# Kernel optimization log

Measured on AMD Instinct MI355X. Metric: run time of the kernel, lower is better.

Reference implementation:

```python
import jax, jax.numpy as jnp
import numpy as np

N_NODES = 50000   # local subgraph nodes
N_ENT   = 100000  # global entity vocab
N_REL   = 16
DIM     = 128
LAYERS  = 2
E       = 600000  # edges
Q       = 8192    # query triples
PATH_DIM = 5
RULE_INIT = [[1.0, 1.0, 0.5, 0.0, 0.0], [0.0, 0.0, 0.0, 1.0, 1.0]]


def setup_inputs() -> dict:
    key = jax.random.key(0)
    ks = jax.random.split(key, 11)
    node_ids   = jax.random.randint(ks[0], (N_NODES,), 0, N_ENT)
    edge_index = jax.random.randint(ks[1], (2, E), 0, N_NODES)
    edge_type  = jax.random.randint(ks[2], (E,), 0, N_REL)
    heads = jax.random.randint(ks[3], (Q,), 0, N_NODES)
    rels  = jax.random.randint(ks[4], (Q,), 0, N_REL)
    tails = jax.random.randint(ks[5], (Q,), 0, N_NODES)
    path_feat = jax.random.normal(ks[6], (Q, PATH_DIM), dtype=jnp.float32)
    # learned parameters
    entity_emb = jax.random.normal(ks[7], (N_ENT, DIM), dtype=jnp.float32) * 0.1
    rel_emb    = jax.random.normal(ks[8], (N_REL, DIM), dtype=jnp.float32) * 0.1
    W_self = jax.random.normal(ks[9], (LAYERS, DIM, DIM), dtype=jnp.float32) / np.sqrt(DIM)
    W_rel  = jax.random.normal(ks[10], (LAYERS, N_REL, DIM, DIM), dtype=jnp.float32) / np.sqrt(DIM)
    delta_weight = jnp.zeros((2, PATH_DIM), dtype=jnp.float32)
    lambda_logit = jnp.zeros((2,), dtype=jnp.float32)
    rule_init_weight = jnp.asarray(RULE_INIT, dtype=jnp.float32)
    return {
        'node_ids': node_ids, 'edge_index': edge_index, 'edge_type': edge_type,
        'heads': heads, 'rels': rels, 'tails': tails,
        'path_feat': path_feat, 'rel_task_idx': 0,
        'entity_emb': entity_emb, 'rel_emb': rel_emb,
        'W_self': W_self, 'W_rel': W_rel,
        'delta_weight': delta_weight, 'lambda_logit': lambda_logit,
        'rule_init_weight': rule_init_weight,
    }


def _rgcn_layer(h, Ws, Wr, src, dst, etype):
    # relation-specific transforms for all nodes: [R, N, D]
    h_rel = jnp.einsum('nd,rde->rne', h, Wr)
    msgs = h_rel[etype, src]                    # [E, D] gather per edge
    # per-(dst, relation) mean normalization (standard RGCN 1/c_{i,r})
    seg = dst * N_REL + etype
    cnt = jax.ops.segment_sum(jnp.ones((E,), h.dtype), seg, num_segments=N_NODES * N_REL)
    msgs = msgs / jnp.maximum(cnt[seg], 1.0)[:, None]
    agg = jax.ops.segment_sum(msgs, dst, num_segments=N_NODES)  # [N, D]
    return jax.nn.relu(h @ Ws + agg)


def reference(node_ids, edge_index, edge_type, heads, rels, tails, path_feat,
              rel_task_idx, entity_emb, rel_emb, W_self, W_rel,
              delta_weight, lambda_logit, rule_init_weight):
    src, dst = edge_index[0], edge_index[1]
    h = entity_emb[node_ids]                      # [N, D] local node states
    for l in range(LAYERS):
        h = _rgcn_layer(h, W_self[l], W_rel[l], src, dst, edge_type)
    # DistMult scoring of query triples (local indices)
    score_graph = jnp.sum(h[heads] * rel_emb[rels] * h[tails], axis=-1)  # [Q]
    # path branch
    final_weight = rule_init_weight[rel_task_idx] + delta_weight[rel_task_idx]  # [PATH_DIM]
    score_path = path_feat @ final_weight                                # [Q]
    lam = jax.nn.sigmoid(lambda_logit[rel_task_idx])
    return lam * score_graph + (1.0 - lam) * score_path
```

## Files before the change

### kernel.cpp

```cpp
#include <hip/hip_runtime.h>

#define N_NODES 50000
#define N_ENT   100000
#define N_REL   16
#define DIM     128
#define E_EDGES 600000
#define NQ      8192
#define PATH_DIM 5
#define NK      (N_NODES * N_REL)
#define NBLK_SEG (NK / 256)
#define KTOT    (N_REL * DIM + DIM)
#define NG      (KTOT / 32)
#define BM      64

typedef __attribute__((ext_vector_type(8))) short short8;
typedef __attribute__((ext_vector_type(4))) float floatx4;

static __device__ __forceinline__ short f2bf(float x) {
  unsigned u = __builtin_bit_cast(unsigned, x);
  u = (u + 0x7FFFu + ((u >> 16) & 1u)) >> 16;
  return (short)u;
}
static __device__ __forceinline__ float bf_lo(unsigned u) {
  return __builtin_bit_cast(float, u << 16);
}
static __device__ __forceinline__ float bf_hi(unsigned u) {
  return __builtin_bit_cast(float, u & 0xffff0000u);
}
static __device__ __forceinline__ unsigned pk2(float a, float b) {
  return (unsigned)(unsigned short)f2bf(a) | ((unsigned)(unsigned short)f2bf(b) << 16);
}

static __device__ __forceinline__ int wave_incl_scan(int x) {
  int lane = threadIdx.x & 63;
  #pragma unroll
  for (int off = 1; off < 64; off <<= 1) {
    int y = __shfl_up(x, off, 64);
    if (lane >= off) x += y;
  }
  return x;
}

__global__ void k_hist(const int* __restrict__ ei, const int* __restrict__ et,
                       int* __restrict__ hist) {
  int e = blockIdx.x * 256 + threadIdx.x;
  if (e >= E_EDGES) return;
  int key = et[e] * N_NODES + ei[E_EDGES + e];
  atomicAdd(&hist[key], 1);
}

__global__ void k_bsum(const int* __restrict__ hist, int* __restrict__ bsum) {
  int t = threadIdx.x;
  int v = hist[blockIdx.x * 256 + t];
  #pragma unroll
  for (int off = 32; off; off >>= 1) v += __shfl_xor(v, off, 64);
  __shared__ int s4[4];
  if ((t & 63) == 0) s4[t >> 6] = v;
  __syncthreads();
  if (t == 0) bsum[blockIdx.x] = s4[0] + s4[1] + s4[2] + s4[3];
}

__global__ void k_bscan(int* __restrict__ bsum) {
  int t = threadIdx.x;
  int v[4], loc[4], s = 0;
  #pragma unroll
  for (int i = 0; i < 4; i++) {
    int idx = t * 4 + i;
    v[i] = (idx < NBLK_SEG) ? bsum[idx] : 0;
    loc[i] = s; s += v[i];
  }
  int incl = wave_incl_scan(s);
  __shared__ int wsum[16];
  int wid = t >> 6, lane = t & 63;
  if (lane == 63) wsum[wid] = incl;
  __syncthreads();
  if (t < 16) {
    int x = wsum[t];
    #pragma unroll
    for (int off = 1; off < 16; off <<= 1) {
      int y = __shfl_up(x, off, 64);
      if (t >= off) x += y;
    }
    wsum[t] = x;
  }
  __syncthreads();
  int wexcl = wid ? wsum[wid - 1] : 0;
  int texcl = wexcl + incl - s;
  #pragma unroll
  for (int i = 0; i < 4; i++) {
    int idx = t * 4 + i;
    if (idx < NBLK_SEG) bsum[idx] = texcl + loc[i];
  }
}

__global__ void k_offsets(const int* __restrict__ hist, const int* __restrict__ bsum,
                          int* __restrict__ offs, int* __restrict__ cursor) {
  int t = threadIdx.x;
  int g = blockIdx.x * 256 + t;
  int v = hist[g];
  int incl = wave_incl_scan(v);
  __shared__ int wsum[4];
  int wid = t >> 6, lane = t & 63;
  if (lane == 63) wsum[wid] = incl;
  __syncthreads();
  int wexcl = 0;
  for (int i = 0; i < wid; i++) wexcl += wsum[i];
  int off = bsum[blockIdx.x] + wexcl + incl - v;
  offs[g] = off;
  cursor[g] = off;
  if (g == NK - 1) offs[NK] = off + v;
}

__global__ void k_scatter(const int* __restrict__ ei, const int* __restrict__ et,
                          int* __restrict__ cursor, int* __restrict__ ssrc) {
  int e = blockIdx.x * 256 + threadIdx.x;
  if (e >= E_EDGES) return;
  int src = ei[e];
  int key = et[e] * N_NODES + ei[E_EDGES + e];
  int pos = atomicAdd(&cursor[key], 1);
  ssrc[pos] = src;
}

__global__ void k_h0(const int* __restrict__ nid, const float* __restrict__ emb,
                     unsigned* __restrict__ h) {
  int g = blockIdx.x * 256 + threadIdx.x;
  int n = g >> 5;
  int q = g & 31;
  float4 v = *(const float4*)(emb + (size_t)nid[n] * DIM + q * 4);
  uint2 pk;
  pk.x = pk2(v.x, v.y);
  pk.y = pk2(v.z, v.w);
  *(uint2*)(h + (size_t)n * 64 + q * 2) = pk;
}

__global__ void k_wcat(const float* __restrict__ wrel, const float* __restrict__ wself,
                       short* __restrict__ wt) {
  int idx = blockIdx.x * 256 + threadIdx.x;
  if (idx >= 2 * NG * 8 * 512) return;
  int within = idx & 511;
  int tile = idx >> 9;
  int rA = within >> 5, q = within & 31;
  int nt8 = tile & 7;
  int lg = tile >> 3;
  int l = lg / NG, g = lg % NG;
  int n = nt8 * 16 + rA;
  int k = g * 32 + q;
  float v;
  if (k < N_REL * DIM) {
    int r = k >> 7, d = k & 127;
    v = wrel[(((size_t)l * N_REL + r) * DIM + d) * DIM + n];
  } else {
    int d = k - N_REL * DIM;
    v = wself[((size_t)l * DIM + d) * DIM + n];
  }
  wt[idx] = f2bf(v);
}

__global__ __launch_bounds__(512, 4) void k_layer(const unsigned* __restrict__ hin,
                                                  const int* __restrict__ offs,
                                                  const int* __restrict__ ssrc,
                                                  const short* __restrict__ wt,
                                                  const unsigned* __restrict__ zrow,
                                                  unsigned* __restrict__ hout) {
  __shared__ unsigned As[2][BM][68];
  __shared__ int offsS[16][66];
  int t = threadIdx.x;
  int w = t >> 6, lane = t & 63;
  int row0 = blockIdx.x * BM;

  for (int idx = t; idx < 16 * 80; idx += 512) {
    int it = idx / 80, r = idx - it * 80;
    if (r < 65) offsS[it][r] = offs[min(it * N_NODES + row0 + r, NK)];
  }
  __syncthreads();

  if (w < 4) {
    int pw = w;
    int seg = lane & 15, edge = lane >> 4;
    int s_l = offsS[0][pw * 16 + seg];
    int e_l = offsS[0][pw * 16 + seg + 1];
    int pfe = ssrc[min(s_l + edge, E_EDGES - 1)];

    auto produce = [&](int buf, int it) {
      int cl = e_l - s_l;
      float invl = 1.0f / (float)(cl > 0 ? cl : 1);
      int invb = __builtin_bit_cast(int, invl);
      unsigned u0[16], u1[16], u2[16], u3[16];
      #pragma unroll
      for (int j = 0; j < 16; ++j) {
        int cnt = __builtin_amdgcn_readlane(cl, j);
        int r0 = __builtin_amdgcn_readlane(pfe, j);
        int r1 = __builtin_amdgcn_readlane(pfe, j + 16);
        int r2 = __builtin_amdgcn_readlane(pfe, j + 32);
        int r3 = __builtin_amdgcn_readlane(pfe, j + 48);
        const unsigned* p0 = (cnt > 0) ? hin + (size_t)r0 * 64 : zrow;
        const unsigned* p1 = (cnt > 1) ? hin + (size_t)r1 * 64 : zrow;
        const unsigned* p2 = (cnt > 2) ? hin + (size_t)r2 * 64 : zrow;
        const unsigned* p3 = (cnt > 3) ? hin + (size_t)r3 * 64 : zrow;
        u0[j] = p0[lane];
        u1[j] = p1[lane];
        u2[j] = p2[lane];
        u3[j] = p3[lane];
      }
      int pfe_n = 0, s_n = 0, e_n = 0;
      if (it < 15) {
        s_n = offsS[it + 1][pw * 16 + seg];
        e_n = offsS[it + 1][pw * 16 + seg + 1];
        pfe_n = ssrc[min(s_n + edge, E_EDGES - 1)];
      }
      __builtin_amdgcn_sched_barrier(0);
      #pragma unroll
      for (int j = 0; j < 16; ++j) {
        int cnt = __builtin_amdgcn_readlane(cl, j);
        float inv = __builtin_bit_cast(float, __builtin_amdgcn_readlane(invb, j));
        float s0 = bf_lo(u0[j]) + bf_lo(u1[j]) + bf_lo(u2[j]) + bf_lo(u3[j]);
        float s1 = bf_hi(u0[j]) + bf_hi(u1[j]) + bf_hi(u2[j]) + bf_hi(u3[j]);
        if (cnt > 4) {
          int sj = __builtin_amdgcn_readlane(s_l, j);
          for (int p = sj + 4; p < sj + cnt; ++p) {
            int sr = __builtin_amdgcn_readfirstlane(ssrc[p]);
            unsigned uu = hin[(size_t)sr * 64 + lane];
            s0 += bf_lo(uu); s1 += bf_hi(uu);
          }
        }
        s0 *= inv; s1 *= inv;
        unsigned pk;
        asm("v_cvt_pk_bf16_f32 %0, %1, %2" : "=v"(pk) : "v"(s0), "v"(s1));
        As[buf][pw * 16 + j][lane] = pk;
      }
      s_l = s_n; e_l = e_n; pfe = pfe_n;
    };

    produce(0, 0);
    __syncthreads();
    for (int it = 0; it < 17; ++it) {
      int nx = it + 1;
      if (nx < 16) {
        produce(nx & 1, nx);
      } else if (nx == 16) {
        #pragma unroll
        for (int j = 0; j < 16; ++j) {
          int lr = min(row0 + pw * 16 + j, N_NODES - 1);
          As[0][pw * 16 + j][lane] = hin[(size_t)lr * 64 + lane];
        }
      }
      __syncthreads();
    }
  } else {
    int wid = w - 4, wm = wid >> 1, wn = wid & 1;
    int quad = lane >> 4, rA = lane & 15;
    floatx4 acc[2][4];
    #pragma unroll
    for (int a = 0; a < 2; a++)
      #pragma unroll
      for (int b = 0; b < 4; b++) acc[a][b] = (floatx4)0.f;

    __syncthreads();
    for (int it = 0; it < 17; ++it) {
      int buf = it & 1;
      const short* arow0 = (const short*)&As[buf][wm * 32 + rA][0];
      const short* arow1 = (const short*)&As[buf][wm * 32 + 16 + rA][0];
      #pragma unroll
      for (int ks = 0; ks < 4; ++ks) {
        short8 a0 = *(const short8*)(arow0 + ks * 32 + quad * 8);
        short8 a1 = *(const short8*)(arow1 + ks * 32 + quad * 8);
        int kg = it * 4 + ks;
        const short* bp = wt + (size_t)(kg * 8 + wn * 4) * 512 + rA * 32 + quad * 8;
        #pragma unroll
        for (int nt = 0; nt < 4; ++nt) {
          short8 b = *(const short8*)(bp + nt * 512);
          acc[0][nt] = __builtin_amdgcn_mfma_f32_16x16x32_bf16(a0, b, acc[0][nt], 0, 0, 0);
          acc[1][nt] = __builtin_amdgcn_mfma_f32_16x16x32_bf16(a1, b, acc[1][nt], 0, 0, 0);
        }
      }
      __syncthreads();
    }
    #pragma unroll
    for (int mt = 0; mt < 2; ++mt)
      #pragma unroll
      for (int nt = 0; nt < 4; ++nt)
        #pragma unroll
        for (int j = 0; j < 4; ++j) {
          int row = row0 + wm * 32 + mt * 16 + quad * 4 + j;
          int col = wn * 64 + nt * 16 + rA;
          if (row < N_NODES)
            ((short*)hout)[(size_t)row * DIM + col] = f2bf(fmaxf(acc[mt][nt][j], 0.f));
        }
  }
}

__global__ void k_score(const unsigned* __restrict__ h, const int* __restrict__ heads,
                        const int* __restrict__ rels, const int* __restrict__ tails,
                        const float* __restrict__ rel_emb, const float* __restrict__ path_feat,
                        const int* __restrict__ task_idx, const float* __restrict__ delta_w,
                        const float* __restrict__ lambda_logit, const float* __restrict__ rule_init,
                        float* __restrict__ out) {
  int q = (blockIdx.x * 256 + threadIdx.x) >> 6;
  int lane = threadIdx.x & 63;
  int hd = heads[q], tl = tails[q], rl = rels[q];
  unsigned ua = h[(size_t)hd * 64 + lane];
  unsigned uc = h[(size_t)tl * 64 + lane];
  float2 r = *(const float2*)(rel_emb + (size_t)rl * DIM + lane * 2);
  float s = bf_lo(ua) * r.x * bf_lo(uc) + bf_hi(ua) * r.y * bf_hi(uc);
  #pragma unroll
  for (int off = 32; off; off >>= 1) s += __shfl_xor(s, off, 64);
  if (lane == 0) {
    int task = task_idx[0];
    float sp = 0.f;
    #pragma unroll
    for (int p = 0; p < PATH_DIM; p++)
      sp += path_feat[q * PATH_DIM + p] *
            (rule_init[task * PATH_DIM + p] + delta_w[task * PATH_DIM + p]);
    float lam = 1.f / (1.f + __expf(-lambda_logit[task]));
    out[q] = lam * s + (1.f - lam) * sp;
  }
}

extern "C" void kernel_launch(void* const* d_in, const int* in_sizes, int n_in,
                              void* d_out, int out_size, void* d_ws, size_t ws_size,
                              hipStream_t stream) {
  const int*   node_ids   = (const int*)d_in[0];
  const int*   edge_index = (const int*)d_in[1];
  const int*   edge_type  = (const int*)d_in[2];
  const int*   heads      = (const int*)d_in[3];
  const int*   rels       = (const int*)d_in[4];
  const int*   tails      = (const int*)d_in[5];
  const float* path_feat  = (const float*)d_in[6];
  const int*   task_idx   = (const int*)d_in[7];
  const float* entity_emb = (const float*)d_in[8];
  const float* rel_emb    = (const float*)d_in[9];
  const float* W_self     = (const float*)d_in[10];
  const float* W_rel      = (const float*)d_in[11];
  const float* delta_w    = (const float*)d_in[12];
  const float* lambda_lg  = (const float*)d_in[13];
  const float* rule_init  = (const float*)d_in[14];

  char* ws = (char*)d_ws;
  size_t off = 0;
  auto alloc = [&](size_t bytes) -> void* {
    void* p = ws + off;
    off = (off + bytes + 255) & ~(size_t)255;
    return p;
  };
  unsigned* h_a    = (unsigned*)alloc((size_t)N_NODES * DIM * 2);
  unsigned* h_b    = (unsigned*)alloc((size_t)N_NODES * DIM * 2);
  short*    wt     = (short*)alloc((size_t)2 * NG * 8 * 512 * 2);
  int*      offs   = (int*)alloc((size_t)(NK + 1) * 4);
  int*      ssrc   = (int*)alloc((size_t)E_EDGES * 4);
  int*      hist   = (int*)alloc((size_t)(NK + 1) * 4);
  int*      cursor = (int*)alloc((size_t)NK * 4);
  int*      bsum   = (int*)alloc((size_t)NBLK_SEG * 4);
  unsigned* zrow   = (unsigned*)alloc(256);

  hipMemsetAsync(hist, 0, (size_t)(NK + 1) * 4, stream);
  hipMemsetAsync(zrow, 0, 256, stream);
  int eb = (E_EDGES + 255) / 256;
  k_hist<<<eb, 256, 0, stream>>>(edge_index, edge_type, hist);
  k_bsum<<<NBLK_SEG, 256, 0, stream>>>(hist, bsum);
  k_bscan<<<1, 1024, 0, stream>>>(bsum);
  k_offsets<<<NBLK_SEG, 256, 0, stream>>>(hist, bsum, offs, cursor);
  k_scatter<<<eb, 256, 0, stream>>>(edge_index, edge_type, cursor, ssrc);
  k_h0<<<(N_NODES * 32) / 256, 256, 0, stream>>>(node_ids, entity_emb, h_a);
  k_wcat<<<(2 * NG * 8 * 512 + 255) / 256, 256, 0, stream>>>(W_rel, W_self, wt);

  const unsigned* hin = h_a;
  unsigned* hout = h_b;
  int nblk = (N_NODES + BM - 1) / BM;
  for (int l = 0; l < 2; l++) {
    k_layer<<<nblk, 512, 0, stream>>>(hin, offs, ssrc,
                                      wt + (size_t)l * NG * 8 * 512, zrow, hout);
    const unsigned* tmp = hout;
    hout = (unsigned*)hin;
    hin = tmp;
  }
  k_score<<<NQ / 4, 256, 0, stream>>>(hin, heads, rels, tails, rel_emb, path_feat,
                                      task_idx, delta_w, lambda_lg, rule_init,
                                      (float*)d_out);
}
```

Measured before the change: 449.3 us.

## Replace CSR build with fixed 4-slot buckets plus overflow linked lists

The histogram, block-sum, scan, offsets and scatter kernels are replaced by a single bucketing kernel. Each (relation, dst) key gets four direct slots, and any further edges go into an atomically allocated overflow linked list. The layer kernel reads counts and slots directly, no longer stages offsets in shared memory, and skips the gathers for empty segments. This removes several preprocessing launches, at the cost of a larger slot array and serial pointer-chasing for high-degree keys. Summation order for overflow edges becomes nondeterministic.

```diff
diff --git a/kernel.cpp b/kernel.cpp
--- a/kernel.cpp
+++ b/kernel.cpp
@@ -8,7 +8,6 @@
 #define NQ      8192
 #define PATH_DIM 5
 #define NK      (N_NODES * N_REL)
-#define NBLK_SEG (NK / 256)
 #define KTOT    (N_REL * DIM + DIM)
 #define NG      (KTOT / 32)
 #define BM      64
@@ -31,94 +30,22 @@
   return (unsigned)(unsigned short)f2bf(a) | ((unsigned)(unsigned short)f2bf(b) << 16);
 }
 
-static __device__ __forceinline__ int wave_incl_scan(int x) {
-  int lane = threadIdx.x & 63;
-  #pragma unroll
-  for (int off = 1; off < 64; off <<= 1) {
-    int y = __shfl_up(x, off, 64);
-    if (lane >= off) x += y;
-  }
-  return x;
-}
-
-__global__ void k_hist(const int* __restrict__ ei, const int* __restrict__ et,
-                       int* __restrict__ hist) {
-  int e = blockIdx.x * 256 + threadIdx.x;
-  if (e >= E_EDGES) return;
-  int key = et[e] * N_NODES + ei[E_EDGES + e];
-  atomicAdd(&hist[key], 1);
-}
-
-__global__ void k_bsum(const int* __restrict__ hist, int* __restrict__ bsum) {
-  int t = threadIdx.x;
-  int v = hist[blockIdx.x * 256 + t];
-  #pragma unroll
-  for (int off = 32; off; off >>= 1) v += __shfl_xor(v, off, 64);
-  __shared__ int s4[4];
-  if ((t & 63) == 0) s4[t >> 6] = v;
-  __syncthreads();
-  if (t == 0) bsum[blockIdx.x] = s4[0] + s4[1] + s4[2] + s4[3];
-}
-
-__global__ void k_bscan(int* __restrict__ bsum) {
-  int t = threadIdx.x;
-  int v[4], loc[4], s = 0;
-  #pragma unroll
-  for (int i = 0; i < 4; i++) {
-    int idx = t * 4 + i;
-    v[i] = (idx < NBLK_SEG) ? bsum[idx] : 0;
-    loc[i] = s; s += v[i];
-  }
-  int incl = wave_incl_scan(s);
-  __shared__ int wsum[16];
-  int wid = t >> 6, lane = t & 63;
-  if (lane == 63) wsum[wid] = incl;
-  __syncthreads();
-  if (t < 16) {
-    int x = wsum[t];
-    #pragma unroll
-    for (int off = 1; off < 16; off <<= 1) {
-      int y = __shfl_up(x, off, 64);
-      if (t >= off) x += y;
-    }
-    wsum[t] = x;
-  }
-  __syncthreads();
-  int wexcl = wid ? wsum[wid - 1] : 0;
-  int texcl = wexcl + incl - s;
-  #pragma unroll
-  for (int i = 0; i < 4; i++) {
-    int idx = t * 4 + i;
-    if (idx < NBLK_SEG) bsum[idx] = texcl + loc[i];
-  }
-}
-
-__global__ void k_offsets(const int* __restrict__ hist, const int* __restrict__ bsum,
-                          int* __restrict__ offs, int* __restrict__ cursor) {
-  int t = threadIdx.x;
-  int g = blockIdx.x * 256 + t;
-  int v = hist[g];
-  int incl = wave_incl_scan(v);
-  __shared__ int wsum[4];
-  int wid = t >> 6, lane = t & 63;
-  if (lane == 63) wsum[wid] = incl;
-  __syncthreads();
-  int wexcl = 0;
-  for (int i = 0; i < wid; i++) wexcl += wsum[i];
-  int off = bsum[blockIdx.x] + wexcl + incl - v;
-  offs[g] = off;
-  cursor[g] = off;
-  if (g == NK - 1) offs[NK] = off + v;
-}
-
-__global__ void k_scatter(const int* __restrict__ ei, const int* __restrict__ et,
-                          int* __restrict__ cursor, int* __restrict__ ssrc) {
+__global__ void k_bucket(const int* __restrict__ ei, const int* __restrict__ et,
+                         int* __restrict__ cnt, int* __restrict__ head,
+                         int* __restrict__ cursor, int* __restrict__ slots,
+                         int* __restrict__ ovf_src, int* __restrict__ ovf_next) {
   int e = blockIdx.x * 256 + threadIdx.x;
   if (e >= E_EDGES) return;
   int src = ei[e];
   int key = et[e] * N_NODES + ei[E_EDGES + e];
-  int pos = atomicAdd(&cursor[key], 1);
-  ssrc[pos] = src;
+  int pos = atomicAdd(&cnt[key], 1);
+  if (pos < 4) {
+    slots[(size_t)key * 4 + pos] = src;
+  } else {
+    int nid = atomicAdd(cursor, 1) + 1;
+    ovf_src[nid] = src;
+    ovf_next[nid] = atomicExch(&head[key], nid);
+  }
 }
 
 __global__ void k_h0(const int* __restrict__ nid, const float* __restrict__ emb,
@@ -157,78 +84,81 @@
 }
 
 __global__ __launch_bounds__(512, 4) void k_layer(const unsigned* __restrict__ hin,
-                                                  const int* __restrict__ offs,
-                                                  const int* __restrict__ ssrc,
+                                                  const int* __restrict__ gcnt,
+                                                  const int* __restrict__ slots,
+                                                  const int* __restrict__ head,
+                                                  const int* __restrict__ ovf_src,
+                                                  const int* __restrict__ ovf_next,
                                                   const short* __restrict__ wt,
                                                   const unsigned* __restrict__ zrow,
                                                   unsigned* __restrict__ hout) {
   __shared__ unsigned As[2][BM][68];
-  __shared__ int offsS[16][66];
   int t = threadIdx.x;
   int w = t >> 6, lane = t & 63;
   int row0 = blockIdx.x * BM;
 
-  for (int idx = t; idx < 16 * 80; idx += 512) {
-    int it = idx / 80, r = idx - it * 80;
-    if (r < 65) offsS[it][r] = offs[min(it * N_NODES + row0 + r, NK)];
-  }
-  __syncthreads();
-
   if (w < 4) {
     int pw = w;
     int seg = lane & 15, edge = lane >> 4;
-    int s_l = offsS[0][pw * 16 + seg];
-    int e_l = offsS[0][pw * 16 + seg + 1];
-    int pfe = ssrc[min(s_l + edge, E_EDGES - 1)];
+    int segbase = row0 + pw * 16;
+    int k0 = min(segbase + seg, NK - 1);
+    int cl  = gcnt[k0];
+    int pfe = slots[(size_t)k0 * 4 + edge];
 
     auto produce = [&](int buf, int it) {
-      int cl = e_l - s_l;
       float invl = 1.0f / (float)(cl > 0 ? cl : 1);
       int invb = __builtin_bit_cast(int, invl);
       unsigned u0[16], u1[16], u2[16], u3[16];
       #pragma unroll
       for (int j = 0; j < 16; ++j) {
-        int cnt = __builtin_amdgcn_readlane(cl, j);
-        int r0 = __builtin_amdgcn_readlane(pfe, j);
-        int r1 = __builtin_amdgcn_readlane(pfe, j + 16);
-        int r2 = __builtin_amdgcn_readlane(pfe, j + 32);
-        int r3 = __builtin_amdgcn_readlane(pfe, j + 48);
-        const unsigned* p0 = (cnt > 0) ? hin + (size_t)r0 * 64 : zrow;
-        const unsigned* p1 = (cnt > 1) ? hin + (size_t)r1 * 64 : zrow;
-        const unsigned* p2 = (cnt > 2) ? hin + (size_t)r2 * 64 : zrow;
-        const unsigned* p3 = (cnt > 3) ? hin + (size_t)r3 * 64 : zrow;
-        u0[j] = p0[lane];
-        u1[j] = p1[lane];
-        u2[j] = p2[lane];
-        u3[j] = p3[lane];
-      }
-      int pfe_n = 0, s_n = 0, e_n = 0;
+        int cj = __builtin_amdgcn_readlane(cl, j);
+        if (cj > 0) {
+          int r0 = __builtin_amdgcn_readlane(pfe, j);
+          int r1 = __builtin_amdgcn_readlane(pfe, j + 16);
+          int r2 = __builtin_amdgcn_readlane(pfe, j + 32);
+          int r3 = __builtin_amdgcn_readlane(pfe, j + 48);
+          const unsigned* p1 = (cj > 1) ? hin + (size_t)r1 * 64 : zrow;
+          const unsigned* p2 = (cj > 2) ? hin + (size_t)r2 * 64 : zrow;
+          const unsigned* p3 = (cj > 3) ? hin + (size_t)r3 * 64 : zrow;
+          u0[j] = hin[(size_t)r0 * 64 + lane];
+          u1[j] = p1[lane];
+          u2[j] = p2[lane];
+          u3[j] = p3[lane];
+        }
+      }
+      int cl_n = 0, pfe_n = 0;
       if (it < 15) {
-        s_n = offsS[it + 1][pw * 16 + seg];
-        e_n = offsS[it + 1][pw * 16 + seg + 1];
-        pfe_n = ssrc[min(s_n + edge, E_EDGES - 1)];
+        int kn = min((it + 1) * N_NODES + segbase + seg, NK - 1);
+        cl_n = gcnt[kn];
+        pfe_n = slots[(size_t)kn * 4 + edge];
       }
       __builtin_amdgcn_sched_barrier(0);
       #pragma unroll
       for (int j = 0; j < 16; ++j) {
-        int cnt = __builtin_amdgcn_readlane(cl, j);
-        float inv = __builtin_bit_cast(float, __builtin_amdgcn_readlane(invb, j));
-        float s0 = bf_lo(u0[j]) + bf_lo(u1[j]) + bf_lo(u2[j]) + bf_lo(u3[j]);
-        float s1 = bf_hi(u0[j]) + bf_hi(u1[j]) + bf_hi(u2[j]) + bf_hi(u3[j]);
-        if (cnt > 4) {
-          int sj = __builtin_amdgcn_readlane(s_l, j);
-          for (int p = sj + 4; p < sj + cnt; ++p) {
-            int sr = __builtin_amdgcn_readfirstlane(ssrc[p]);
-            unsigned uu = hin[(size_t)sr * 64 + lane];
-            s0 += bf_lo(uu); s1 += bf_hi(uu);
+        int cj = __builtin_amdgcn_readlane(cl, j);
+        if (cj == 0) {
+          As[buf][pw * 16 + j][lane] = 0u;
+        } else {
+          float inv = __builtin_bit_cast(float, __builtin_amdgcn_readlane(invb, j));
+          float s0 = bf_lo(u0[j]) + bf_lo(u1[j]) + bf_lo(u2[j]) + bf_lo(u3[j]);
+          float s1 = bf_hi(u0[j]) + bf_hi(u1[j]) + bf_hi(u2[j]) + bf_hi(u3[j]);
+          if (cj > 4) {
+            int kj = min(it * N_NODES + segbase + j, NK - 1);
+            int cur = __builtin_amdgcn_readfirstlane(head[kj]);
+            for (int x = 4; x < cj; ++x) {
+              int sr = __builtin_amdgcn_readfirstlane(ovf_src[cur]);
+              unsigned uu = hin[(size_t)sr * 64 + lane];
+              s0 += bf_lo(uu); s1 += bf_hi(uu);
+              cur = __builtin_amdgcn_readfirstlane(ovf_next[cur]);
+            }
           }
-        }
-        s0 *= inv; s1 *= inv;
-        unsigned pk;
-        asm("v_cvt_pk_bf16_f32 %0, %1, %2" : "=v"(pk) : "v"(s0), "v"(s1));
-        As[buf][pw * 16 + j][lane] = pk;
-      }
-      s_l = s_n; e_l = e_n; pfe = pfe_n;
+          s0 *= inv; s1 *= inv;
+          unsigned pk;
+          asm("v_cvt_pk_bf16_f32 %0, %1, %2" : "=v"(pk) : "v"(s0), "v"(s1));
+          As[buf][pw * 16 + j][lane] = pk;
+        }
+      }
+      cl = cl_n; pfe = pfe_n;
     };
 
     produce(0, 0);
@@ -240,7 +170,7 @@
       } else if (nx == 16) {
         #pragma unroll
         for (int j = 0; j < 16; ++j) {
-          int lr = min(row0 + pw * 16 + j, N_NODES - 1);
+          int lr = min(segbase + j, N_NODES - 1);
           As[0][pw * 16 + j][lane] = hin[(size_t)lr * 64 + lane];
         }
       }
@@ -345,21 +275,20 @@
   unsigned* h_a    = (unsigned*)alloc((size_t)N_NODES * DIM * 2);
   unsigned* h_b    = (unsigned*)alloc((size_t)N_NODES * DIM * 2);
   short*    wt     = (short*)alloc((size_t)2 * NG * 8 * 512 * 2);
-  int*      offs   = (int*)alloc((size_t)(NK + 1) * 4);
-  int*      ssrc   = (int*)alloc((size_t)E_EDGES * 4);
-  int*      hist   = (int*)alloc((size_t)(NK + 1) * 4);
-  int*      cursor = (int*)alloc((size_t)NK * 4);
-  int*      bsum   = (int*)alloc((size_t)NBLK_SEG * 4);
+  int*      zreg   = (int*)alloc((size_t)(2 * NK + 64) * 4);
+  int*      cntA   = zreg;
+  int*      headA  = zreg + NK;
+  int*      cursor = zreg + 2 * NK;
+  int*      slots  = (int*)alloc((size_t)NK * 4 * 4);
+  int*      ovf_s  = (int*)alloc((size_t)(E_EDGES + 2) * 4);
+  int*      ovf_n  = (int*)alloc((size_t)(E_EDGES + 2) * 4);
   unsigned* zrow   = (unsigned*)alloc(256);
 
-  hipMemsetAsync(hist, 0, (size_t)(NK + 1) * 4, stream);
+  hipMemsetAsync(zreg, 0, (size_t)(2 * NK + 64) * 4, stream);
   hipMemsetAsync(zrow, 0, 256, stream);
   int eb = (E_EDGES + 255) / 256;
-  k_hist<<<eb, 256, 0, stream>>>(edge_index, edge_type, hist);
-  k_bsum<<<NBLK_SEG, 256, 0, stream>>>(hist, bsum);
-  k_bscan<<<1, 1024, 0, stream>>>(bsum);
-  k_offsets<<<NBLK_SEG, 256, 0, stream>>>(hist, bsum, offs, cursor);
-  k_scatter<<<eb, 256, 0, stream>>>(edge_index, edge_type, cursor, ssrc);
+  k_bucket<<<eb, 256, 0, stream>>>(edge_index, edge_type, cntA, headA, cursor,
+                                   slots, ovf_s, ovf_n);
   k_h0<<<(N_NODES * 32) / 256, 256, 0, stream>>>(node_ids, entity_emb, h_a);
   k_wcat<<<(2 * NG * 8 * 512 + 255) / 256, 256, 0, stream>>>(W_rel, W_self, wt);
 
@@ -367,7 +296,7 @@
   unsigned* hout = h_b;
   int nblk = (N_NODES + BM - 1) / BM;
   for (int l = 0; l < 2; l++) {
-    k_layer<<<nblk, 512, 0, stream>>>(hin, offs, ssrc,
+    k_layer<<<nblk, 512, 0, stream>>>(hin, cntA, slots, headA, ovf_s, ovf_n,
                                       wt + (size_t)l * NG * 8 * 512, zrow, hout);
     const unsigned* tmp = hout;
     hout = (unsigned*)hin;
```

Result: slower. 508.3 us (+13.1%).
